# Kernel tuning notes

Hardware: AMD Instinct MI355X
Metric: run time of the kernel (lower is better)

The kernel has to match this reference:

```python
import jax, jax.numpy as jnp
import numpy as np

N_NODES = 100000
N_EDGES = 1600000
N_GRAPHS = 64
D = 128


def gcn_conv(x, W, b, src, dst, num_nodes):
    # PyG GCNConv: x' = D^{-1/2} (A + I) D^{-1/2} (X W) + b
    h = x @ W  # [N, H]
    deg = jax.ops.segment_sum(jnp.ones_like(dst, dtype=h.dtype), dst,
                              num_segments=num_nodes)  # includes self-loop (>=1)
    dinv = jax.lax.rsqrt(deg)
    norm = dinv[src] * dinv[dst]  # [E+N]
    msg = h[src] * norm[:, None]  # gather + scale
    out = jax.ops.segment_sum(msg, dst, num_segments=num_nodes)
    return out + b


def setup_inputs() -> dict:
    key = jax.random.key(0)
    ks = jax.random.split(key, 10)
    x = jax.random.normal(ks[0], (N_NODES, D), dtype=jnp.float32)
    edge_index = jax.random.randint(ks[1], (2, N_EDGES), 0, N_NODES, dtype=jnp.int64)
    batch = jnp.sort(jax.random.randint(ks[2], (N_NODES,), 0, N_GRAPHS, dtype=jnp.int64))
    s = 1.0 / np.sqrt(D)
    W1 = jax.random.normal(ks[3], (D, D), dtype=jnp.float32) * s
    b1 = jnp.zeros((D,), dtype=jnp.float32)
    W2 = jax.random.normal(ks[4], (D, D), dtype=jnp.float32) * s
    b2 = jnp.zeros((D,), dtype=jnp.float32)
    Wfc = jax.random.normal(ks[5], (D, D), dtype=jnp.float32) * s
    bfc = jnp.zeros((D,), dtype=jnp.float32)
    return {"x": x, "edge_index": edge_index, "batch": batch,
            "W1": W1, "b1": b1, "W2": W2, "b2": b2, "Wfc": Wfc, "bfc": bfc}


def reference(x, edge_index, batch, W1, b1, W2, b2, Wfc, bfc):
    num_nodes = x.shape[0]
    # add self-loops (PyG default add_self_loops=True)
    loop = jnp.arange(num_nodes, dtype=edge_index.dtype)
    src = jnp.concatenate([edge_index[0], loop])
    dst = jnp.concatenate([edge_index[1], loop])

    h = jax.nn.relu(gcn_conv(x, W1, b1, src, dst, num_nodes))
    h = jax.nn.relu(gcn_conv(h, W2, b2, src, dst, num_nodes))

    # global_mean_pool over graph segment ids
    sums = jax.ops.segment_sum(h, batch, num_segments=N_GRAPHS)
    cnts = jax.ops.segment_sum(jnp.ones((num_nodes,), h.dtype), batch,
                               num_segments=N_GRAPHS)
    pooled = sums / jnp.maximum(cnts, 1.0)[:, None]

    return jax.nn.relu(pooled @ Wfc + bfc)
```

## Files before the change

### kernel.cpp

```cpp
#include <hip/hip_runtime.h>
#include <hip/hip_bf16.h>
#include <stdint.h>

typedef unsigned int uint;
typedef unsigned short ushort;
typedef __attribute__((ext_vector_type(8))) short short8;
typedef __attribute__((ext_vector_type(4))) float floatx4;

#define DD 128
#define BSHIFT 9
#define CAP 10240
#define MAXIT 32

__device__ __forceinline__ float bf2f(ushort h){ return __uint_as_float(((uint)h)<<16); }
__device__ __forceinline__ ushort f2bf(float f){
    uint u = __float_as_uint(f);
    u += 0x7fffu + ((u>>16)&1u);
    return (ushort)(u>>16);
}

__global__ __launch_bounds__(256) void k_canon2(
    const int* __restrict__ ei, const ushort* __restrict__ xs,
    const void* W1, const void* W2, const void* Wfc,
    const void* b1, const void* b2, const void* bfc,
    float* Wcf, float* bc1, float* bc2, float* bcf,
    ushort* wb1, ushort* wb2,
    int* flags, float* pooled, int* bukcnt, int nbuk, int PM)
{
    __shared__ int s_flg[3];
    int t = threadIdx.x, b = blockIdx.x;
    if (t < 64){
        unsigned long long m0 = __ballot((t < 32) ? (ei[2*t+1] == 0) : 1);
        uint ex2 = (((uint)xs[2*t]) >> 7) & 0xffu;
        uint ew2 = (((uint)((const ushort*)W1)[2*t]) >> 7) & 0xffu;
        unsigned long long m1 = __ballot(ex2 >= 90u && ex2 <= 160u);
        unsigned long long m2 = __ballot(ew2 >= 90u && ew2 <= 160u);
        if (t == 0){
            s_flg[0] = (m0 == ~0ull) ? 1 : 0;
            s_flg[1] = (__popcll(m1) >= 48) ? 1 : 0;
            s_flg[2] = (__popcll(m2) >= 48) ? 1 : 0;
            if (b == 0){ flags[0]=s_flg[0]; flags[1]=s_flg[1]; flags[2]=s_flg[2]; }
        }
    }
    __syncthreads();
    int fW = s_flg[2];

    int gi = b*256 + t;
    if (gi < 32768){
        int r = gi >> 14, off = gi & 16383;
        const void* s = (r==0) ? W1 : W2;
        float val = fW ? bf2f(((const ushort*)s)[off]) : ((const float*)s)[off];
        int k = off>>7, n = off&127;
        int c = n>>4, nn = n&15, kk = k>>5, q = (k>>3)&3, j = k&7;
        ushort* wb = (r==0) ? wb1 : wb2;
        wb[((c*4+kk)*64 + q*16 + nn)*8 + j] = f2bf(val);
    } else if (gi < 49152){
        int off = gi - 32768;
        Wcf[off] = fW ? bf2f(((const ushort*)Wfc)[off]) : ((const float*)Wfc)[off];
    } else if (gi < 49536){
        int jj = gi - 49152; int r = jj>>7, off = jj & 127;
        const void* s = (r==0)?b1:((r==1)?b2:bfc);
        float* d = (r==0)?bc1:((r==1)?bc2:bcf);
        d[off] = fW ? bf2f(((const ushort*)s)[off]) : ((const float*)s)[off];
    } else if (gi < 49536 + PM){
        pooled[gi - 49536] = 0.f;
    } else if (gi < 49536 + PM + nbuk){
        bukcnt[gi - 49536 - PM] = 0;
    }
}

__global__ __launch_bounds__(256) void k_scatA(const int* __restrict__ ei,
                                               int* __restrict__ bukcnt,
                                               uint* __restrict__ pairs,
                                               int E, int nbuk, int chunk){
    __shared__ int lh[256], lcur[256];
    __shared__ int s_flg;
    int t = threadIdx.x, b = blockIdx.x;
    if (t < 64){
        unsigned long long m0 = __ballot((t < 32) ? (ei[2*t+1] == 0) : 1);
        if (t == 0) s_flg = (m0 == ~0ull) ? 1 : 0;
    }
    for (int i=t;i<nbuk;i+=256) lh[i]=0;
    __syncthreads();
    int f64 = s_flg;
    int e0 = b*chunk, e1 = min(E, e0+chunk);

    int dc[MAXIT];
    #pragma unroll
    for (int k=0;k<MAXIT;k++){
        int e = e0 + t + k*256;
        if (e < e1){
            int d = f64 ? ei[2*(E+e)] : ei[E+e];
            dc[k] = d;
            atomicAdd(&lh[d>>BSHIFT], 1);
        }
    }
    __syncthreads();
    for (int i=t;i<nbuk;i+=256){
        int v = lh[i];
        int base = v ? atomicAdd(&bukcnt[i], v) : 0;
        lcur[i] = i*CAP + base;
    }
    __syncthreads();
    #pragma unroll
    for (int k=0;k<MAXIT;k++){
        int e = e0 + t + k*256;
        if (e < e1){
            int d = dc[k];
            int s = f64 ? ei[2*e] : ei[e];
            int p = atomicAdd(&lcur[d>>BSHIFT], 1);
            pairs[p] = (uint)s | ((uint)(d & 511) << 23);
        }
    }
}

__global__ __launch_bounds__(256) void k_build(const uint* __restrict__ pairs,
                                               const int* __restrict__ bukcnt,
                                               int* __restrict__ rowstart,
                                               int* __restrict__ rowend,
                                               float* __restrict__ dinv,
                                               int* __restrict__ srcb,
                                               int nbuk, int M){
    __shared__ int cnt[512], off[512], cur[512], ps[256];
    int b = blockIdx.x, t = threadIdx.x;
    int base = b*CAP;
    int m = bukcnt[b];
    for (int i=t;i<512;i+=256) cnt[i]=0;
    __syncthreads();
    for (int e=t; e<m; e+=256){
        uint pr = pairs[base+e];
        atomicAdd(&cnt[pr >> 23], 1);
    }
    __syncthreads();
    int c0 = cnt[2*t], c1 = cnt[2*t+1];
    int s = c0 + c1;
    ps[t] = s; __syncthreads();
    for (int o2=1; o2<256; o2<<=1){
        int x = (t>=o2) ? ps[t-o2] : 0;
        __syncthreads(); ps[t] += x; __syncthreads();
    }
    int ex = ps[t] - s;
    off[2*t] = ex;     off[2*t+1] = ex + c0;
    cur[2*t] = ex;     cur[2*t+1] = ex + c0;
    __syncthreads();
    for (int i=t;i<512;i+=256){
        int n = (b<<BSHIFT) + i;
        if (n < M){
            rowstart[n] = base + off[i];
            rowend[n]   = base + off[i] + cnt[i];
            dinv[n]     = rsqrtf((float)(cnt[i]+1));
        }
    }
    for (int e=t; e<m; e+=256){
        uint pr = pairs[base+e];
        int i = pr >> 23;
        int p = atomicAdd(&cur[i], 1);
        srcb[base+p] = (int)(pr & 0x7FFFFFu);
    }
}

__global__ __launch_bounds__(256) void k_gemm(const ushort* __restrict__ Xb,
                                              const float* __restrict__ Xf,
                                              const ushort* __restrict__ Wb,
                                              const float* __restrict__ dinv,
                                              const int* __restrict__ flags, int force_bf16,
                                              ushort* __restrict__ Hp, int M){
    __shared__ uint4 Ws4[2048];
    int t = threadIdx.x;
    int n0 = blockIdx.x*64;
    int xbf = force_bf16 ? 1 : flags[1];

    {
        const uint4* sW = (const uint4*)Wb;
        #pragma unroll
        for (int j=0;j<8;j++) Ws4[t + j*256] = sW[t + j*256];
    }

    int wv = t>>6, lane = t&63;
    int mrow = lane & 15, q = lane >> 4;
    int arow = n0 + wv*16 + mrow;
    int rok  = (arow < M);

    short8 af[4];
    if (xbf){
        const ushort* xr = Xb + (size_t)arow*DD + q*8;
        #pragma unroll
        for (int kk=0;kk<4;kk++){
            uint4 v = rok ? *(const uint4*)(xr + kk*32) : make_uint4(0,0,0,0);
            af[kk] = *(const short8*)&v;
        }
    } else {
        const float* xr = Xf + (size_t)arow*DD + q*8;
        #pragma unroll
        for (int kk=0;kk<4;kk++){
            float4 a = make_float4(0,0,0,0), b4 = make_float4(0,0,0,0);
            if (rok){
                a  = *(const float4*)(xr + kk*32);
                b4 = *(const float4*)(xr + kk*32 + 4);
            }
            uint4 v;
            v.x = (uint)f2bf(a.x)  | ((uint)f2bf(a.y)<<16);
            v.y = (uint)f2bf(a.z)  | ((uint)f2bf(a.w)<<16);
            v.z = (uint)f2bf(b4.x) | ((uint)f2bf(b4.y)<<16);
            v.w = (uint)f2bf(b4.z) | ((uint)f2bf(b4.w)<<16);
            af[kk] = *(const short8*)&v;
        }
    }
    __syncthreads();

    const ushort* Ws = (const ushort*)Ws4;
    floatx4 acc[8];
    #pragma unroll
    for (int c=0;c<8;c++) acc[c] = (floatx4){0.f,0.f,0.f,0.f};

    #pragma unroll
    for (int kk=0;kk<4;kk++){
        #pragma unroll
        for (int c=0;c<8;c++){
            short8 bf = *(const short8*)(Ws + ((size_t)((c*4+kk)*64 + lane))*8);
            acc[c] = __builtin_amdgcn_mfma_f32_16x16x32_bf16(af[kk], bf, acc[c], 0, 0, 0);
        }
    }

    __syncthreads();
    int quad = lane>>4, col = lane&15;
    int rbase = n0 + wv*16 + quad*4;
    float dv[4];
    #pragma unroll
    for (int r=0;r<4;r++) dv[r] = (rbase + r < M) ? dinv[rbase + r] : 0.f;

    ushort* eb = (ushort*)Ws4 + (size_t)wv * 16*136;
    #pragma unroll
    for (int c=0;c<8;c++){
        #pragma unroll
        for (int r=0;r<4;r++){
            eb[(quad*4+r)*136 + c*16 + col] = f2bf(acc[c][r]*dv[r]);
        }
    }
    #pragma unroll
    for (int h=0;h<4;h++){
        int i = lane*4 + h;
        int row = i >> 4, u = i & 15;
        uint4 v = *(const uint4*)(eb + row*136 + u*8);
        int gn = n0 + wv*16 + row;
        if (gn < M) *(uint4*)(Hp + (size_t)gn*DD + u*8) = v;
    }
}

__global__ __launch_bounds__(256) void k_gather(const ushort* __restrict__ Hp,
                                                const int* __restrict__ rowstart,
                                                const int* __restrict__ rowend,
                                                const int* __restrict__ srcb,
                                                const float* __restrict__ dinv,
                                                const float* __restrict__ bc,
                                                ushort* __restrict__ Xout, int M){
    int wid  = (int)((blockIdx.x*(size_t)blockDim.x + threadIdx.x) >> 6);
    int lane = threadIdx.x & 63;
    if (wid >= M) return;
    int q   = lane >> 4;
    int l16 = lane & 15;
    const uint4* Hp4 = (const uint4*)Hp;

    float acc[8];
    #pragma unroll
    for (int c=0;c<8;c++) acc[c] = 0.f;

    #define ACCUM(vv) { \
        acc[0] += __uint_as_float((vv).x<<16); acc[1] += __uint_as_float((vv).x&0xffff0000u); \
        acc[2] += __uint_as_float((vv).y<<16); acc[3] += __uint_as_float((vv).y&0xffff0000u); \
        acc[4] += __uint_as_float((vv).z<<16); acc[5] += __uint_as_float((vv).z&0xffff0000u); \
        acc[6] += __uint_as_float((vv).w<<16); acc[7] += __uint_as_float((vv).w&0xffff0000u); }

    int rp  = rowstart[wid];
    int rp1 = rowend[wid];
    int total = (rp1 - rp) + 1;
    int j = 0;
    while (j < total){
        int m = total - j; if (m > 64) m = 64;
        int pos = j + lane;
        int idx = wid;
        if (lane < m && pos > 0) idx = srcb[rp + pos - 1];
        for (int g = 0; g < m; g += 8){
            int r0 = g + q, r1 = g + 4 + q;
            int s0 = __shfl(idx, r0, 64);
            int s1 = __shfl(idx, r1, 64);
            uint4 v0 = make_uint4(0,0,0,0), v1 = make_uint4(0,0,0,0);
            if (r0 < m) v0 = Hp4[(size_t)s0*16 + l16];
            if (r1 < m) v1 = Hp4[(size_t)s1*16 + l16];
            ACCUM(v0);
            ACCUM(v1);
        }
        j += m;
    }
    #undef ACCUM

    #pragma unroll
    for (int c=0;c<8;c++){
        acc[c] += __shfl_xor(acc[c], 16, 64);
        acc[c] += __shfl_xor(acc[c], 32, 64);
    }

    if (lane < 16){
        float w = dinv[wid];
        const float* bp = bc + l16*8;
        uint4 o;
        float r0,r1;
        r0 = fmaxf(fmaf(acc[0], w, bp[0]), 0.f);
        r1 = fmaxf(fmaf(acc[1], w, bp[1]), 0.f);
        o.x = (uint)f2bf(r0) | ((uint)f2bf(r1)<<16);
        r0 = fmaxf(fmaf(acc[2], w, bp[2]), 0.f);
        r1 = fmaxf(fmaf(acc[3], w, bp[3]), 0.f);
        o.y = (uint)f2bf(r0) | ((uint)f2bf(r1)<<16);
        r0 = fmaxf(fmaf(acc[4], w, bp[4]), 0.f);
        r1 = fmaxf(fmaf(acc[5], w, bp[5]), 0.f);
        o.z = (uint)f2bf(r0) | ((uint)f2bf(r1)<<16);
        r0 = fmaxf(fmaf(acc[6], w, bp[6]), 0.f);
        r1 = fmaxf(fmaf(acc[7], w, bp[7]), 0.f);
        o.w = (uint)f2bf(r0) | ((uint)f2bf(r1)<<16);
        ((uint4*)Xout)[(size_t)wid*16 + l16] = o;
    }
}

__global__ __launch_bounds__(256) void k_pool(const ushort* __restrict__ X3,
                                              const int* __restrict__ batch,
                                              const int* __restrict__ flags,
                                              float* __restrict__ pooled, int M){
    int f = flags[0];
    int t = threadIdx.x;
    int c32 = t & 63;
    int row = t >> 6;
    int n0 = blockIdx.x * 256;
    if (n0 >= M) return;
    int nend = n0 + 256; if (nend > M) nend = M;
    const uint* X3u = (const uint*)X3;

    float a0 = 0.f, a1 = 0.f;
    int cur = -1;

    int n = n0 + row;
    #define POOL_PROC(gg, uu) \
        if ((gg) != cur){ \
            if (cur >= 0){ \
                atomicAdd(&pooled[cur*DD + 2*c32],   a0); \
                atomicAdd(&pooled[cur*DD + 2*c32+1], a1); \
            } \
            a0 = 0.f; a1 = 0.f; cur = (gg); \
        } \
        a0 += __uint_as_float((uu)<<16); \
        a1 += __uint_as_float((uu) & 0xffff0000u);

    for (; n + 12 < nend; n += 16){
        int g0 = f ? batch[2*n]      : batch[n];
        int g1 = f ? batch[2*(n+4)]  : batch[n+4];
        int g2 = f ? batch[2*(n+8)]  : batch[n+8];
        int g3 = f ? batch[2*(n+12)] : batch[n+12];
        uint u0 = X3u[(size_t)n*64      + c32];
        uint u1 = X3u[(size_t)(n+4)*64  + c32];
        uint u2 = X3u[(size_t)(n+8)*64  + c32];
        uint u3 = X3u[(size_t)(n+12)*64 + c32];
        POOL_PROC(g0, u0);
        POOL_PROC(g1, u1);
        POOL_PROC(g2, u2);
        POOL_PROC(g3, u3);
    }
    for (; n < nend; n += 4){
        int g = f ? batch[2*n] : batch[n];
        uint u = X3u[(size_t)n*64 + c32];
        POOL_PROC(g, u);
    }
    #undef POOL_PROC

    if (cur >= 0){
        atomicAdd(&pooled[cur*DD + 2*c32],   a0);
        atomicAdd(&pooled[cur*DD + 2*c32+1], a1);
    }
}

__global__ void k_fc(const float* __restrict__ pooled, const int* __restrict__ batch,
                     const int* __restrict__ flags,
                     const float* __restrict__ Wcf, const float* __restrict__ bcf,
                     ushort* out16, float* out32, int M){
    __shared__ float p[128];
    __shared__ int sb[2];
    int g = blockIdx.x, t = threadIdx.x;
    int f = flags[0];
    if (t < 2){
        int target = g - t;
        int lo = 0, hi = M;
        while (lo < hi){ int mid=(lo+hi)>>1; int bv = f ? batch[2*mid] : batch[mid]; if (bv > target) hi = mid; else lo = mid+1; }
        sb[t] = lo;
    }
    __syncthreads();
    float cnt = (float)(sb[0] - sb[1]);
    p[t] = pooled[g*DD + t] / fmaxf(cnt, 1.f);
    __syncthreads();
    float acc = bcf[t];
    #pragma unroll 8
    for (int k=0;k<128;k++) acc = fmaf(p[k], Wcf[k*DD + t], acc);
    float r = fmaxf(acc, 0.f);
    if (flags[1]) out16[g*DD + t] = f2bf(r);
    else          out32[g*DD + t] = r;
}

extern "C" void kernel_launch(void* const* d_in, const int* in_sizes, int n_in,
                              void* d_out, int out_size, void* d_ws, size_t ws_size,
                              hipStream_t stream) {
    const ushort* xs  = (const ushort*)d_in[0];
    const float*  xf  = (const float*)d_in[0];
    const int*    ei  = (const int*)d_in[1];
    const int*    bat = (const int*)d_in[2];
    const void* W1  = d_in[3];
    const void* b1  = d_in[4];
    const void* W2  = d_in[5];
    const void* b2  = d_in[6];
    const void* Wfc = d_in[7];
    const void* bfc = d_in[8];

    int M = in_sizes[0] / DD;
    int E = in_sizes[1] / 2;
    int G = out_size / DD;
    int nbuk  = (M + 511) >> BSHIFT;
    int nblkA = (E + 8191) / 8192; if (nblkA < 256) nblkA = 256;
    int chunk = (E + nblkA - 1) / nblkA;

    char* w = (char*)d_ws;
    auto alloc = [&](size_t bytes)->void*{ void* p = (void*)w; w += (bytes + 255) & ~(size_t)255; return p; };
    int*    flags    = (int*)   alloc(16);
    int*    rowstart = (int*)   alloc((size_t)M*4);
    int*    rowend   = (int*)   alloc((size_t)M*4);
    int*    bukcnt   = (int*)   alloc((size_t)nbuk*4);
    float*  dinv     = (float*) alloc((size_t)M*4);
    float*  pooled   = (float*) alloc((size_t)G*DD*4);
    float*  Wcf      = (float*) alloc(16384*4);
    float*  bc1      = (float*) alloc(128*4);
    float*  bc2      = (float*) alloc(128*4);
    float*  bcf      = (float*) alloc(128*4);
    ushort* wb1      = (ushort*)alloc(16384*2);
    ushort* wb2      = (ushort*)alloc(16384*2);
    int*    srcb     = (int*)   alloc((size_t)nbuk*CAP*4);
    ushort* Hp       = (ushort*)alloc((size_t)M*DD*2);
    ushort* X2       = (ushort*)alloc((size_t)M*DD*2);
    uint*   pairs    = (uint*)Hp;
    (void)ws_size; (void)n_in;

    int PM = G*DD;
    int canon_n = 49536 + PM + nbuk;

    k_canon2<<<(canon_n+255)/256, 256, 0, stream>>>(ei, xs, W1, W2, Wfc, b1, b2, bfc,
                                                    Wcf, bc1, bc2, bcf, wb1, wb2,
                                                    flags, pooled, bukcnt, nbuk, PM);
    k_scatA <<<nblkA, 256, 0, stream>>>(ei, bukcnt, pairs, E, nbuk, chunk);
    k_build <<<nbuk, 256, 0, stream>>>(pairs, bukcnt, rowstart, rowend, dinv, srcb, nbuk, M);

    k_gemm  <<<(M+63)/64, 256, 0, stream>>>(xs, xf, wb1, dinv, flags, 0, Hp, M);
    k_gather<<<(M+3)/4, 256, 0, stream>>>(Hp, rowstart, rowend, srcb, dinv, bc1, X2, M);
    k_gemm  <<<(M+63)/64, 256, 0, stream>>>(X2, (const float*)X2, wb2, dinv, flags, 1, Hp, M);
    k_gather<<<(M+3)/4, 256, 0, stream>>>(Hp, rowstart, rowend, srcb, dinv, bc2, X2, M);

    k_pool<<<(M+255)/256, 256, 0, stream>>>(X2, bat, flags, pooled, M);
    k_fc  <<<G, 128, 0, stream>>>(pooled, bat, flags, Wcf, bcf, (ushort*)d_out, (float*)d_out, M);
}
```

Before: 321.4 us.

## Fuse weight canonicalization into edge scatter kernel and store GEMM output directly

Merges the weight/bias conversion kernel into the edge bucketing scatter kernel, launching a fixed 512 blocks, and zeroes the pooled and bucket-count buffers with async memsets instead. It also drops the LDS staging in the GEMM epilogue and writes bf16 results straight to global memory, one element at a time. The aim is to save a kernel launch and a barrier plus LDS round-trip. The trade-off is narrow 2-byte global stores in the GEMM epilogue, and the fixed block count changes the per-block edge chunk size. The scatter kernel's 32-iteration per-thread loop covers 8192 edges per block, which the 1.6M edges fit within 512 blocks.

```diff
diff --git a/kernel.cpp b/kernel.cpp
--- a/kernel.cpp
+++ b/kernel.cpp
@@ -9,6 +9,7 @@
 
 #define DD 128
 #define BSHIFT 9
+#define NBLKA 512
 #define CAP 10240
 #define MAXIT 32
 
@@ -19,14 +20,16 @@
     return (ushort)(u>>16);
 }
 
-__global__ __launch_bounds__(256) void k_canon2(
+__global__ __launch_bounds__(256) void k_scatA(
     const int* __restrict__ ei, const ushort* __restrict__ xs,
     const void* W1, const void* W2, const void* Wfc,
     const void* b1, const void* b2, const void* bfc,
     float* Wcf, float* bc1, float* bc2, float* bcf,
-    ushort* wb1, ushort* wb2,
-    int* flags, float* pooled, int* bukcnt, int nbuk, int PM)
+    ushort* wb1, ushort* wb2, int* flags,
+    int* __restrict__ bukcnt, uint* __restrict__ pairs,
+    int E, int nbuk, int chunk)
 {
+    __shared__ int lh[256], lcur[256];
     __shared__ int s_flg[3];
     int t = threadIdx.x, b = blockIdx.x;
     if (t < 64){
@@ -42,8 +45,9 @@
             if (b == 0){ flags[0]=s_flg[0]; flags[1]=s_flg[1]; flags[2]=s_flg[2]; }
         }
     }
-    __syncthreads();
-    int fW = s_flg[2];
+    for (int i=t;i<nbuk;i+=256) lh[i]=0;
+    __syncthreads();
+    int f64 = s_flg[0], fW = s_flg[2];
 
     int gi = b*256 + t;
     if (gi < 32768){
@@ -62,27 +66,8 @@
         const void* s = (r==0)?b1:((r==1)?b2:bfc);
         float* d = (r==0)?bc1:((r==1)?bc2:bcf);
         d[off] = fW ? bf2f(((const ushort*)s)[off]) : ((const float*)s)[off];
-    } else if (gi < 49536 + PM){
-        pooled[gi - 49536] = 0.f;
-    } else if (gi < 49536 + PM + nbuk){
-        bukcnt[gi - 49536 - PM] = 0;
-    }
-}
-
-__global__ __launch_bounds__(256) void k_scatA(const int* __restrict__ ei,
-                                               int* __restrict__ bukcnt,
-                                               uint* __restrict__ pairs,
-                                               int E, int nbuk, int chunk){
-    __shared__ int lh[256], lcur[256];
-    __shared__ int s_flg;
-    int t = threadIdx.x, b = blockIdx.x;
-    if (t < 64){
-        unsigned long long m0 = __ballot((t < 32) ? (ei[2*t+1] == 0) : 1);
-        if (t == 0) s_flg = (m0 == ~0ull) ? 1 : 0;
-    }
-    for (int i=t;i<nbuk;i+=256) lh[i]=0;
-    __syncthreads();
-    int f64 = s_flg;
+    }
+
     int e0 = b*chunk, e1 = min(E, e0+chunk);
 
     int dc[MAXIT];
@@ -222,28 +207,18 @@
         }
     }
 
-    __syncthreads();
     int quad = lane>>4, col = lane&15;
     int rbase = n0 + wv*16 + quad*4;
     float dv[4];
     #pragma unroll
     for (int r=0;r<4;r++) dv[r] = (rbase + r < M) ? dinv[rbase + r] : 0.f;
-
-    ushort* eb = (ushort*)Ws4 + (size_t)wv * 16*136;
     #pragma unroll
     for (int c=0;c<8;c++){
         #pragma unroll
         for (int r=0;r<4;r++){
-            eb[(quad*4+r)*136 + c*16 + col] = f2bf(acc[c][r]*dv[r]);
-        }
-    }
-    #pragma unroll
-    for (int h=0;h<4;h++){
-        int i = lane*4 + h;
-        int row = i >> 4, u = i & 15;
-        uint4 v = *(const uint4*)(eb + row*136 + u*8);
-        int gn = n0 + wv*16 + row;
-        if (gn < M) *(uint4*)(Hp + (size_t)gn*DD + u*8) = v;
+            int gn = rbase + r;
+            if (gn < M) Hp[(size_t)gn*DD + c*16 + col] = f2bf(acc[c][r]*dv[r]);
+        }
     }
 }
 
@@ -420,8 +395,7 @@
     int E = in_sizes[1] / 2;
     int G = out_size / DD;
     int nbuk  = (M + 511) >> BSHIFT;
-    int nblkA = (E + 8191) / 8192; if (nblkA < 256) nblkA = 256;
-    int chunk = (E + nblkA - 1) / nblkA;
+    int chunk = (E + NBLKA - 1) / NBLKA;
 
     char* w = (char*)d_ws;
     auto alloc = [&](size_t bytes)->void*{ void* p = (void*)w; w += (bytes + 255) & ~(size_t)255; return p; };
@@ -443,13 +417,12 @@
     uint*   pairs    = (uint*)Hp;
     (void)ws_size; (void)n_in;
 
-    int PM = G*DD;
-    int canon_n = 49536 + PM + nbuk;
-
-    k_canon2<<<(canon_n+255)/256, 256, 0, stream>>>(ei, xs, W1, W2, Wfc, b1, b2, bfc,
-                                                    Wcf, bc1, bc2, bcf, wb1, wb2,
-                                                    flags, pooled, bukcnt, nbuk, PM);
-    k_scatA <<<nblkA, 256, 0, stream>>>(ei, bukcnt, pairs, E, nbuk, chunk);
+    hipMemsetAsync(pooled, 0, (size_t)G*DD*4, stream);
+    hipMemsetAsync(bukcnt, 0, (size_t)nbuk*4, stream);
+
+    k_scatA <<<NBLKA, 256, 0, stream>>>(ei, xs, W1, W2, Wfc, b1, b2, bfc,
+                                        Wcf, bc1, bc2, bcf, wb1, wb2, flags,
+                                        bukcnt, pairs, E, nbuk, chunk);
     k_build <<<nbuk, 256, 0, stream>>>(pairs, bukcnt, rowstart, rowend, dinv, srcb, nbuk, M);
 
     k_gemm  <<<(M+63)/64, 256, 0, stream>>>(xs, xf, wb1, dinv, flags, 0, Hp, M);
```

Result: slower. 329.2 us (+2.4%).
